# Kernel optimization log

Hardware: AMD Instinct MI355X
Metric: run time of the kernel (lower is better)

## Reference

```python
import jax, jax.numpy as jnp
import numpy as np

N = 100000   # nodes
E = 600000   # edges
G = 512      # graphs in batch
EPS = 1e-5   # LayerNorm eps
IN_DIM = 60 + 2 + 12  # dyn feats*frames + dims + st embedding
H = 128


def setup_inputs() -> dict:
    key = jax.random.key(0)
    ks = jax.random.split(key, 32)
    inp = {
        "x": jax.random.normal(ks[0], (N, 60), jnp.float32),
        "xdims": jax.random.uniform(ks[1], (N, 2), jnp.float32),
        "xsttype": jax.random.randint(ks[2], (N,), 0, 256, jnp.int32),
        "edge_index": jax.random.randint(ks[3], (2, E), 0, N, jnp.int32),
        "batch": jnp.sort(jax.random.randint(ks[4], (N,), 0, G, jnp.int32)),
        "emb": jax.random.normal(ks[5], (256, 12), jnp.float32),
    }
    def lin(k, i, o):
        s = 1.0 / np.sqrt(i)
        return jax.random.uniform(k, (i, o), jnp.float32, -s, s)
    dims = [IN_DIM, H, H]
    for l in range(2):
        i, o = dims[l], dims[l + 1]
        inp[f"Wl{l}"] = lin(ks[6 + 4 * l], i, o)   # lin_l: applied to aggregated neighbors
        inp[f"bl{l}"] = jnp.zeros((o,), jnp.float32)
        inp[f"Wr{l}"] = lin(ks[7 + 4 * l], i, o)   # lin_r: applied to root (no bias, PyG SAGEConv)
        inp[f"g{l}"] = jnp.ones((o,), jnp.float32)   # LayerNorm gamma
        inp[f"bn{l}"] = jnp.zeros((o,), jnp.float32)  # LayerNorm beta
    ld = [2 * H, 50, 50, 10]
    for l in range(3):
        inp[f"Wf{l}"] = lin(ks[20 + l], ld[l], ld[l + 1])
        inp[f"bf{l}"] = jnp.zeros((ld[l + 1],), jnp.float32)
    return inp


def _layer_norm(h, g, b):
    mu = jnp.mean(h, axis=-1, keepdims=True)
    var = jnp.mean(jnp.square(h - mu), axis=-1, keepdims=True)
    return (h - mu) * jax.lax.rsqrt(var + EPS) * g + b


def reference(x, xdims, xsttype, edge_index, batch, emb,
              Wl0, bl0, Wr0, g0, bn0,
              Wl1, bl1, Wr1, g1, bn1,
              Wf0, bf0, Wf1, bf1, Wf2, bf2):
    # node feature assembly: [N, 60+2+12]
    h = jnp.concatenate([x, xdims, emb[xsttype]], axis=1)

    src, dst = edge_index[0], edge_index[1]
    deg = jax.ops.segment_sum(jnp.ones((E,), h.dtype), dst, num_segments=N)
    inv_deg = (1.0 / jnp.maximum(deg, 1.0))[:, None]

    for Wl, bl, Wr, g, bn in ((Wl0, bl0, Wr0, g0, bn0), (Wl1, bl1, Wr1, g1, bn1)):
        # SAGEConv (mean aggr): out = lin_l(mean_j x_j) + lin_r(x_i)
        agg = jax.ops.segment_sum(h[src], dst, num_segments=N) * inv_deg
        h = agg @ Wl + bl + h @ Wr
        h = jax.nn.relu(_layer_norm(h, g, bn))  # dropout inactive (eval)

    # global mean / max pooling over graphs
    cnt = jax.ops.segment_sum(jnp.ones((N,), h.dtype), batch, num_segments=G)
    xmean = jax.ops.segment_sum(h, batch, num_segments=G) / jnp.maximum(cnt, 1.0)[:, None]
    xmax = jax.ops.segment_max(h, batch, num_segments=G)
    z = jnp.concatenate([xmean, xmax], axis=1)  # [G, 2H]

    for Wf, bf in ((Wf0, bf0), (Wf1, bf1), (Wf2, bf2)):
        z = jax.nn.relu(z @ Wf + bf)  # Linear + ReLU + Dropout(eval)
    return z
```

## Files before the change

kernel.cpp:

```cpp
#include <hip/hip_runtime.h>

#define NN 100000
#define NP 100096
#define NT (NP / 32)
#define EE 600000
#define GG 512
#define LN_EPS 1e-5f

typedef __attribute__((ext_vector_type(8))) __bf16 bf16x8;
typedef __attribute__((ext_vector_type(4))) float f32x4;

__device__ __forceinline__ unsigned short f2bf(float f) {
    unsigned int u = __float_as_uint(f);
    u = (u + 0x7fffu + ((u >> 16) & 1u)) >> 16;
    return (unsigned short)u;
}
__device__ __forceinline__ unsigned int pack2(float a, float b) {
    return (unsigned int)f2bf(a) | ((unsigned int)f2bf(b) << 16);
}
__device__ __forceinline__ void acc8(float* s, uint4 v) {
    s[0] += __uint_as_float(v.x << 16);
    s[1] += __uint_as_float(v.x & 0xffff0000u);
    s[2] += __uint_as_float(v.y << 16);
    s[3] += __uint_as_float(v.y & 0xffff0000u);
    s[4] += __uint_as_float(v.z << 16);
    s[5] += __uint_as_float(v.z & 0xffff0000u);
    s[6] += __uint_as_float(v.w << 16);
    s[7] += __uint_as_float(v.w & 0xffff0000u);
}

#define PREP_A (NP * 10)
#define PREP_W0 (128 * 160)
#define PREP_W1 (128 * 256)
#define PREP_WF (50 * 256 + 50 * 50 + 50 * 10)
#define PREP_TOT (PREP_A + PREP_W0 + PREP_W1 + PREP_WF + EE)

__global__ __launch_bounds__(256) void prep_kernel(
    const float* __restrict__ x, const float* __restrict__ xdims,
    const int* __restrict__ stt, const float* __restrict__ emb,
    const int* __restrict__ ei,
    const float* __restrict__ Wl0, const float* __restrict__ Wr0,
    const float* __restrict__ Wl1, const float* __restrict__ Wr1,
    const float* __restrict__ Wf0, const float* __restrict__ Wf1,
    const float* __restrict__ Wf2,
    unsigned short* __restrict__ H0r,
    unsigned short* __restrict__ Wt0, unsigned short* __restrict__ Wt1,
    float* __restrict__ W0T, float* __restrict__ W1T, float* __restrict__ W2T,
    int* __restrict__ deg)
{
    int idx = blockIdx.x * 256 + threadIdx.x;
    if (idx < PREP_A) {
        int node = idx / 10;
        int c8 = (idx - node * 10) * 8;
        unsigned short vals[8];
        if (node < NN) {
            int st = stt[node];
            #pragma unroll
            for (int i = 0; i < 8; ++i) {
                int f = c8 + i;
                float v = 0.f;
                if (f < 60)      v = x[node * 60 + f];
                else if (f < 62) v = xdims[node * 2 + (f - 60)];
                else if (f < 74) v = emb[st * 12 + (f - 62)];
                vals[i] = f2bf(v);
            }
        } else {
            #pragma unroll
            for (int i = 0; i < 8; ++i) vals[i] = 0;
        }
        uint4 o;
        o.x = (unsigned)vals[0] | ((unsigned)vals[1] << 16);
        o.y = (unsigned)vals[2] | ((unsigned)vals[3] << 16);
        o.z = (unsigned)vals[4] | ((unsigned)vals[5] << 16);
        o.w = (unsigned)vals[6] | ((unsigned)vals[7] << 16);
        *(uint4*)(H0r + (size_t)node * 80 + c8) = o;
    } else if (idx < PREP_A + PREP_W0) {
        int j = idx - PREP_A;
        int n = j / 160, k = j - n * 160;
        float v = 0.f;
        if (k < 74)                  v = Wl0[k * 128 + n];
        else if (k >= 80 && k < 154) v = Wr0[(k - 80) * 128 + n];
        Wt0[(size_t)n * 160 + k] = f2bf(v);
    } else if (idx < PREP_A + PREP_W0 + PREP_W1) {
        int j = idx - PREP_A - PREP_W0;
        int n = j >> 8, k = j & 255;
        float v = (k < 128) ? Wl1[k * 128 + n] : Wr1[(k - 128) * 128 + n];
        Wt1[(size_t)n * 256 + k] = f2bf(v);
    } else if (idx < PREP_A + PREP_W0 + PREP_W1 + PREP_WF) {
        int j = idx - PREP_A - PREP_W0 - PREP_W1;
        if (j < 50 * 256) {
            int t = j >> 8, k = j & 255;
            W0T[t * 256 + k] = Wf0[k * 50 + t];
        } else if (j < 50 * 256 + 50 * 50) {
            int q = j - 50 * 256; int t = q / 50, k = q - t * 50;
            W1T[t * 50 + k] = Wf1[k * 50 + t];
        } else {
            int q = j - 50 * 256 - 50 * 50; int t = q / 50, k = q - t * 50;
            W2T[t * 50 + k] = Wf2[k * 10 + t];
        }
    } else if (idx < PREP_TOT) {
        int e = idx - PREP_A - PREP_W0 - PREP_W1 - PREP_WF;
        atomicAdd(&deg[ei[EE + e]], 1);
    }
}

__global__ __launch_bounds__(256) void scan1_kernel(
    const int* __restrict__ deg, int* __restrict__ offs, int* __restrict__ bsum)
{
    __shared__ int ts[256];
    int t = threadIdx.x;
    int base = blockIdx.x * 2048 + t * 8;
    int d[8];
    if (base + 8 <= NN) {
        int4 a = *(const int4*)&deg[base];
        int4 b = *(const int4*)&deg[base + 4];
        d[0]=a.x; d[1]=a.y; d[2]=a.z; d[3]=a.w;
        d[4]=b.x; d[5]=b.y; d[6]=b.z; d[7]=b.w;
    } else {
        #pragma unroll
        for (int i = 0; i < 8; ++i) d[i] = (base + i < NN) ? deg[base + i] : 0;
    }
    int e[8]; int run = 0;
    #pragma unroll
    for (int i = 0; i < 8; ++i) { e[i] = run; run += d[i]; }
    ts[t] = run;
    int tot = run;
    __syncthreads();
    for (int off = 1; off < 256; off <<= 1) {
        int u = (t >= off) ? ts[t - off] : 0;
        __syncthreads();
        ts[t] += u;
        __syncthreads();
    }
    int pre = ts[t] - tot;
    #pragma unroll
    for (int i = 0; i < 8; ++i) if (base + i < NN) offs[base + i] = e[i] + pre;
    if (t == 255) bsum[blockIdx.x] = ts[255];
}

__global__ void scan2_kernel(int* __restrict__ bsum, int nb)
{
    int t = threadIdx.x;
    int v = (t < nb) ? bsum[t] : 0;
    int inc = v;
    for (int off = 1; off < 64; off <<= 1) {
        int u = __shfl_up(inc, off, 64);
        if (t >= off) inc += u;
    }
    if (t < nb) bsum[t] = inc - v;
}

__global__ __launch_bounds__(256) void fill_csr_kernel(
    const int* __restrict__ ei, int* __restrict__ cur,
    const int* __restrict__ offs, const int* __restrict__ bsum,
    int* __restrict__ csr)
{
    int e = blockIdx.x * 256 + threadIdx.x;
    if (e >= EE) return;
    int d = ei[EE + e];
    int p = offs[d] + bsum[d >> 11] + atomicAdd(&cur[d], 1);
    csr[p] = ei[e];
}

template<int K, bool POOL>
__global__ __launch_bounds__(256, 4) void gemm_kernel(
    const unsigned short* __restrict__ Hr,
    const unsigned short* __restrict__ Wt,
    const float* __restrict__ bias, const float* __restrict__ gamma,
    const float* __restrict__ beta,
    unsigned short* __restrict__ outH,
    const int* __restrict__ batch,
    float* __restrict__ psum, int* __restrict__ pmax, int* __restrict__ gcnt,
    const int* __restrict__ csr, const int* __restrict__ offs,
    const int* __restrict__ bsum, const int* __restrict__ deg)
{
    constexpr int KT = K / 32, AS = K + 8, KH = K / 2, CH = KH / 8;
    constexpr int SMEM = (32 * AS * 2 > 32 * 128 * 4) ? 32 * AS * 2 : 32 * 128 * 4;
    __shared__ __align__(16) char smem[SMEM];
    unsigned short* Asm = (unsigned short*)smem;
    float* Hs = (float*)smem;
    __shared__ __align__(16) float sP[32 * 4];
    __shared__ __align__(16) float qP[32 * 4];
    __shared__ int bS[POOL ? 32 : 1];

    const int tid = threadIdx.x;
    const int n0 = blockIdx.x * 32;
    const int l = tid & 63, w = tid >> 6;
    const int fg = l >> 4, c0 = l & 15;

    if (POOL && tid < 32) {
        int gn = n0 + tid;
        bS[tid] = (gn < NN) ? batch[gn] : -1;
    }
    float bia[2], gam[2], bet[2];
    #pragma unroll
    for (int j = 0; j < 2; ++j) {
        int col = (2 * w + j) * 16 + c0;
        bia[j] = bias[col]; gam[j] = gamma[col]; bet[j] = beta[col];
    }
    const unsigned short* bp0 = Wt + (size_t)((2 * w + 0) * 16 + c0) * K + fg * 8;
    const unsigned short* bp1 = Wt + (size_t)((2 * w + 1) * 16 + c0) * K + fg * 8;

    {
        const int ln = tid & 15, nl = tid >> 4;
        #pragma unroll
        for (int half = 0; half < 2; ++half) {
            int node = half * 16 + nl;
            int gn = n0 + node;
            if (ln < CH) {
                uint4 rv = *(const uint4*)(Hr + (size_t)gn * KH + ln * 8);
                int d = 0, st = 0;
                if (gn < NN) { d = deg[gn]; st = offs[gn] + bsum[gn >> 11]; }
                float iv = 1.0f / (float)(d > 1 ? d : 1);
                float s[8];
                #pragma unroll
                for (int i = 0; i < 8; ++i) s[i] = 0.f;
                int e = 0;
                for (; e + 4 <= d; e += 4) {
                    int i0 = csr[st + e],     i1 = csr[st + e + 1];
                    int i2 = csr[st + e + 2], i3 = csr[st + e + 3];
                    uint4 v0 = *(const uint4*)(Hr + (size_t)i0 * KH + ln * 8);
                    uint4 v1 = *(const uint4*)(Hr + (size_t)i1 * KH + ln * 8);
                    uint4 v2 = *(const uint4*)(Hr + (size_t)i2 * KH + ln * 8);
                    uint4 v3 = *(const uint4*)(Hr + (size_t)i3 * KH + ln * 8);
                    acc8(s, v0); acc8(s, v1); acc8(s, v2); acc8(s, v3);
                }
                for (; e < d; ++e) {
                    int i0 = csr[st + e];
                    uint4 v0 = *(const uint4*)(Hr + (size_t)i0 * KH + ln * 8);
                    acc8(s, v0);
                }
                uint4 o;
                o.x = pack2(s[0] * iv, s[1] * iv);
                o.y = pack2(s[2] * iv, s[3] * iv);
                o.z = pack2(s[4] * iv, s[5] * iv);
                o.w = pack2(s[6] * iv, s[7] * iv);
                *(uint4*)(Asm + node * AS + ln * 8) = o;
                *(uint4*)(Asm + node * AS + KH + ln * 8) = rv;
            }
        }
    }

    const unsigned short* ar0 = Asm + (0 * 16 + c0) * AS + fg * 8;
    const unsigned short* ar1 = Asm + (1 * 16 + c0) * AS + fg * 8;
    __syncthreads();

    f32x4 acc[2][2];
    acc[0][0] = (f32x4){0.f,0.f,0.f,0.f}; acc[0][1] = (f32x4){0.f,0.f,0.f,0.f};
    acc[1][0] = (f32x4){0.f,0.f,0.f,0.f}; acc[1][1] = (f32x4){0.f,0.f,0.f,0.f};

    #pragma unroll
    for (int kt = 0; kt < KT; ++kt) {
        bf16x8 b0 = *(const bf16x8*)(bp0 + kt * 32);
        bf16x8 b1 = *(const bf16x8*)(bp1 + kt * 32);
        bf16x8 a0 = *(const bf16x8*)(ar0 + kt * 32);
        bf16x8 a1 = *(const bf16x8*)(ar1 + kt * 32);
        acc[0][0] = __builtin_amdgcn_mfma_f32_16x16x32_bf16(a0, b0, acc[0][0], 0, 0, 0);
        acc[0][1] = __builtin_amdgcn_mfma_f32_16x16x32_bf16(a0, b1, acc[0][1], 0, 0, 0);
        acc[1][0] = __builtin_amdgcn_mfma_f32_16x16x32_bf16(a1, b0, acc[1][0], 0, 0, 0);
        acc[1][1] = __builtin_amdgcn_mfma_f32_16x16x32_bf16(a1, b1, acc[1][1], 0, 0, 0);
    }

    #pragma unroll
    for (int m = 0; m < 2; ++m) {
        #pragma unroll
        for (int r = 0; r < 4; ++r) {
            float h0v = acc[m][0][r] + bia[0];
            float h1v = acc[m][1][r] + bia[1];
            float s = h0v + h1v, q = h0v * h0v + h1v * h1v;
            #pragma unroll
            for (int mm = 1; mm < 16; mm <<= 1) {
                s += __shfl_xor(s, mm, 64);
                q += __shfl_xor(q, mm, 64);
            }
            if (c0 == 0) {
                int node = m * 16 + fg * 4 + r;
                sP[node * 4 + w] = s;
                qP[node * 4 + w] = q;
            }
        }
    }
    __syncthreads();

    #pragma unroll
    for (int m = 0; m < 2; ++m) {
        #pragma unroll
        for (int r = 0; r < 4; ++r) {
            int node = m * 16 + fg * 4 + r;
            float4 sv = *(const float4*)&sP[node * 4];
            float4 qv = *(const float4*)&qP[node * 4];
            float s = (sv.x + sv.y) + (sv.z + sv.w);
            float q = (qv.x + qv.y) + (qv.z + qv.w);
            float mu   = s * (1.f / 128.f);
            float var  = q * (1.f / 128.f) - mu * mu;
            float rinv = rsqrtf(var + LN_EPS);
            float h0v = acc[m][0][r] + bia[0];
            float h1v = acc[m][1][r] + bia[1];
            float v0 = fmaxf(0.f, (h0v - mu) * rinv * gam[0] + bet[0]);
            float v1 = fmaxf(0.f, (h1v - mu) * rinv * gam[1] + bet[1]);
            if (POOL) {
                Hs[node * 128 + (2 * w) * 16 + c0]     = v0;
                Hs[node * 128 + (2 * w + 1) * 16 + c0] = v1;
            } else {
                size_t gn = (size_t)(n0 + node);
                float keep = (gn < (size_t)NN) ? 1.f : 0.f;
                outH[gn * 128 + (2 * w) * 16 + c0]     = f2bf(v0 * keep);
                outH[gn * 128 + (2 * w + 1) * 16 + c0] = f2bf(v1 * keep);
            }
        }
    }
    if (!POOL) return;
    __syncthreads();

    if (tid < 128) {
        int j = tid;
        int curg = -1; float s = 0.f, m = 0.f; int rl = 0;
        #pragma unroll 4
        for (int n = 0; n < 32; ++n) {
            int gb = bS[n];
            if (gb < 0) break;
            if (gb != curg) {
                if (curg >= 0) {
                    atomicAdd(&psum[curg * 128 + j], s);
                    atomicMax(&pmax[curg * 128 + j], __float_as_int(m));
                    if (j == 0) atomicAdd(&gcnt[curg], rl);
                }
                curg = gb; s = 0.f; m = 0.f; rl = 0;
            }
            float v = Hs[n * 128 + j];
            s += v; m = fmaxf(m, v);
            rl += 1;
        }
        if (curg >= 0) {
            atomicAdd(&psum[curg * 128 + j], s);
            atomicMax(&pmax[curg * 128 + j], __float_as_int(m));
            if (j == 0) atomicAdd(&gcnt[curg], rl);
        }
    }
}

__global__ __launch_bounds__(64) void mlp_kernel(
    const float* __restrict__ psum, const int* __restrict__ pmax,
    const int* __restrict__ gcnt,
    const float* __restrict__ W0T, const float* __restrict__ bf0,
    const float* __restrict__ W1T, const float* __restrict__ bf1,
    const float* __restrict__ W2T, const float* __restrict__ bf2,
    float* __restrict__ out)
{
    __shared__ float z[256];
    __shared__ float t1[50];
    __shared__ float t2[50];
    int g = blockIdx.x, t = threadIdx.x;
    int c = gcnt[g];
    float ic = 1.0f / (float)(c > 1 ? c : 1);
    for (int j = t; j < 128; j += 64) {
        z[j]       = psum[g * 128 + j] * ic;
        z[128 + j] = __int_as_float(pmax[g * 128 + j]);
    }
    __syncthreads();
    if (t < 50) {
        const float* wr = W0T + t * 256;
        float a0 = bf0[t], a1 = 0.f, a2 = 0.f, a3 = 0.f;
        for (int k = 0; k < 256; k += 4) {
            float4 wv = *(const float4*)(wr + k);
            a0 = fmaf(z[k],     wv.x, a0);
            a1 = fmaf(z[k + 1], wv.y, a1);
            a2 = fmaf(z[k + 2], wv.z, a2);
            a3 = fmaf(z[k + 3], wv.w, a3);
        }
        t1[t] = fmaxf((a0 + a1) + (a2 + a3), 0.0f);
    }
    __syncthreads();
    if (t < 50) {
        const float* wr = W1T + t * 50;
        float a0 = bf1[t], a1 = 0.f;
        for (int k = 0; k < 50; k += 2) {
            a0 = fmaf(t1[k],     wr[k],     a0);
            a1 = fmaf(t1[k + 1], wr[k + 1], a1);
        }
        t2[t] = fmaxf(a0 + a1, 0.0f);
    }
    __syncthreads();
    if (t < 10) {
        const float* wr = W2T + t * 50;
        float a0 = bf2[t], a1 = 0.f;
        for (int k = 0; k < 50; k += 2) {
            a0 = fmaf(t2[k],     wr[k],     a0);
            a1 = fmaf(t2[k + 1], wr[k + 1], a1);
        }
        out[g * 10 + t] = fmaxf(a0 + a1, 0.0f);
    }
}

extern "C" void kernel_launch(void* const* d_in, const int* in_sizes, int n_in,
                              void* d_out, int out_size, void* d_ws, size_t ws_size,
                              hipStream_t stream)
{
    const float* x     = (const float*)d_in[0];
    const float* xdims = (const float*)d_in[1];
    const int*   stt   = (const int*)d_in[2];
    const int*   ei    = (const int*)d_in[3];
    const int*   batch = (const int*)d_in[4];
    const float* emb   = (const float*)d_in[5];
    const float* Wl0   = (const float*)d_in[6];
    const float* bl0   = (const float*)d_in[7];
    const float* Wr0   = (const float*)d_in[8];
    const float* g0    = (const float*)d_in[9];
    const float* bn0   = (const float*)d_in[10];
    const float* Wl1   = (const float*)d_in[11];
    const float* bl1   = (const float*)d_in[12];
    const float* Wr1   = (const float*)d_in[13];
    const float* g1    = (const float*)d_in[14];
    const float* bn1   = (const float*)d_in[15];
    const float* Wf0   = (const float*)d_in[16];
    const float* bf0   = (const float*)d_in[17];
    const float* Wf1   = (const float*)d_in[18];
    const float* bf1   = (const float*)d_in[19];
    const float* Wf2   = (const float*)d_in[20];
    const float* bf2   = (const float*)d_in[21];

    char* w = (char*)d_ws;
    unsigned short* H0r = (unsigned short*)w; w += (size_t)NP * 80 * 2;
    unsigned short* H1  = (unsigned short*)w; w += (size_t)NP * 128 * 2;
    unsigned short* Wt0 = (unsigned short*)w; w += (size_t)128 * 160 * 2;
    unsigned short* Wt1 = (unsigned short*)w; w += (size_t)128 * 256 * 2;
    float* W0T = (float*)w; w += (size_t)50 * 256 * 4;
    float* W1T = (float*)w; w += (size_t)50 * 50 * 4;
    float* W2T = (float*)w; w += (size_t)10 * 50 * 4;
    int*   csr    = (int*)w;   w += (size_t)EE * 4;
    int*   offs   = (int*)w;   w += (size_t)NN * 4;
    int*   bsum   = (int*)w;   w += 1024;
    char* zbeg = w;
    int*   deg  = (int*)w;   w += (size_t)NP * 4;
    int*   cur  = (int*)w;   w += (size_t)NN * 4;
    float* psum = (float*)w; w += (size_t)GG * 128 * 4;
    int*   pmax = (int*)w;   w += (size_t)GG * 128 * 4;
    int*   gcnt = (int*)w;   w += (size_t)GG * 4;
    size_t zsz = (size_t)(w - zbeg);

    hipMemsetAsync(zbeg, 0, zsz, stream);

    prep_kernel<<<(PREP_TOT + 255) / 256, 256, 0, stream>>>(
        x, xdims, stt, emb, ei, Wl0, Wr0, Wl1, Wr1, Wf0, Wf1, Wf2,
        H0r, Wt0, Wt1, W0T, W1T, W2T, deg);

    int nb = (NN + 2047) / 2048;
    scan1_kernel<<<nb, 256, 0, stream>>>(deg, offs, bsum);
    scan2_kernel<<<1, 64, 0, stream>>>(bsum, nb);
    fill_csr_kernel<<<(EE + 255) / 256, 256, 0, stream>>>(ei, cur, offs, bsum, csr);

    gemm_kernel<160, false><<<NT, 256, 0, stream>>>(
        H0r, Wt0, bl0, g0, bn0, H1, nullptr, nullptr, nullptr, nullptr,
        csr, offs, bsum, deg);
    gemm_kernel<256, true><<<NT, 256, 0, stream>>>(
        H1, Wt1, bl1, g1, bn1, nullptr, batch, psum, pmax, gcnt,
        csr, offs, bsum, deg);

    mlp_kernel<<<GG, 64, 0, stream>>>(psum, pmax, gcnt, W0T, bf0, W1T, bf1, W2T, bf2,
                                      (float*)d_out);
}
```

Before: 277.8 us.

## Partition degree count and CSR fill by destination range to localize atomics

The degree-count atomics in prep and the CSR fill kernel now have each edge chunk read by 8 blocks. Each block only handles destinations inside its own 12500-node partition. The aim is to keep the atomic targets and scattered writes of concurrently running blocks within a narrower address range, for better cache and L2 locality, and to vectorize the edge-index loads. The cost is that every edge-index chunk is read 8 times and most lanes idle through the branch checks.

```diff
diff --git a/kernel.cpp b/kernel.cpp
--- a/kernel.cpp
+++ b/kernel.cpp
@@ -33,7 +33,15 @@
 #define PREP_W0 (128 * 160)
 #define PREP_W1 (128 * 256)
 #define PREP_WF (50 * 256 + 50 * 50 + 50 * 10)
-#define PREP_TOT (PREP_A + PREP_W0 + PREP_W1 + PREP_WF + EE)
+#define PREP_AB   (PREP_A / 256)
+#define PREP_W0B  (PREP_W0 / 256)
+#define PREP_W1B  (PREP_W1 / 256)
+#define PREP_WFB  ((PREP_WF + 255) / 256)
+#define PREP_FIXED_B (PREP_AB + PREP_W0B + PREP_W1B + PREP_WFB)
+#define ECHUNK 2048
+#define NCHUNK ((EE + ECHUNK - 1) / ECHUNK)
+#define PREP_GRID (PREP_FIXED_B + NCHUNK * 8)
+#define PART 12500
 
 __global__ __launch_bounds__(256) void prep_kernel(
     const float* __restrict__ x, const float* __restrict__ xdims,
@@ -48,7 +56,28 @@
     float* __restrict__ W0T, float* __restrict__ W1T, float* __restrict__ W2T,
     int* __restrict__ deg)
 {
-    int idx = blockIdx.x * 256 + threadIdx.x;
+    int blk = blockIdx.x;
+    if (blk >= PREP_FIXED_B) {
+        int eb = blk - PREP_FIXED_B;
+        int px = eb & 7, c = eb >> 3;
+        int lo = px * PART, hi = lo + PART;
+        int base = c * ECHUNK + threadIdx.x * 8;
+        int d[8]; int n = 0;
+        if (base + 8 <= EE) {
+            int4 a = *(const int4*)&ei[EE + base];
+            int4 b = *(const int4*)&ei[EE + base + 4];
+            d[0]=a.x; d[1]=a.y; d[2]=a.z; d[3]=a.w;
+            d[4]=b.x; d[5]=b.y; d[6]=b.z; d[7]=b.w;
+            n = 8;
+        } else {
+            for (int u = 0; u < 8 && base + u < EE; ++u) d[u] = ei[EE + base + u];
+            n = (base < EE) ? (EE - base < 8 ? EE - base : 8) : 0;
+        }
+        for (int u = 0; u < n; ++u)
+            if (d[u] >= lo && d[u] < hi) atomicAdd(&deg[d[u]], 1);
+        return;
+    }
+    int idx = blk * 256 + threadIdx.x;
     if (idx < PREP_A) {
         int node = idx / 10;
         int c8 = (idx - node * 10) * 8;
@@ -86,7 +115,7 @@
         int n = j >> 8, k = j & 255;
         float v = (k < 128) ? Wl1[k * 128 + n] : Wr1[(k - 128) * 128 + n];
         Wt1[(size_t)n * 256 + k] = f2bf(v);
-    } else if (idx < PREP_A + PREP_W0 + PREP_W1 + PREP_WF) {
+    } else {
         int j = idx - PREP_A - PREP_W0 - PREP_W1;
         if (j < 50 * 256) {
             int t = j >> 8, k = j & 255;
@@ -94,13 +123,10 @@
         } else if (j < 50 * 256 + 50 * 50) {
             int q = j - 50 * 256; int t = q / 50, k = q - t * 50;
             W1T[t * 50 + k] = Wf1[k * 50 + t];
-        } else {
+        } else if (j < PREP_WF) {
             int q = j - 50 * 256 - 50 * 50; int t = q / 50, k = q - t * 50;
             W2T[t * 50 + k] = Wf2[k * 10 + t];
         }
-    } else if (idx < PREP_TOT) {
-        int e = idx - PREP_A - PREP_W0 - PREP_W1 - PREP_WF;
-        atomicAdd(&deg[ei[EE + e]], 1);
     }
 }
 
@@ -155,11 +181,27 @@
     const int* __restrict__ offs, const int* __restrict__ bsum,
     int* __restrict__ csr)
 {
-    int e = blockIdx.x * 256 + threadIdx.x;
-    if (e >= EE) return;
-    int d = ei[EE + e];
-    int p = offs[d] + bsum[d >> 11] + atomicAdd(&cur[d], 1);
-    csr[p] = ei[e];
+    int px = blockIdx.x & 7, c = blockIdx.x >> 3;
+    int lo = px * PART, hi = lo + PART;
+    int base = c * ECHUNK + threadIdx.x * 8;
+    int d[8]; int n = 0;
+    if (base + 8 <= EE) {
+        int4 a = *(const int4*)&ei[EE + base];
+        int4 b = *(const int4*)&ei[EE + base + 4];
+        d[0]=a.x; d[1]=a.y; d[2]=a.z; d[3]=a.w;
+        d[4]=b.x; d[5]=b.y; d[6]=b.z; d[7]=b.w;
+        n = 8;
+    } else {
+        for (int u = 0; u < 8 && base + u < EE; ++u) d[u] = ei[EE + base + u];
+        n = (base < EE) ? (EE - base < 8 ? EE - base : 8) : 0;
+    }
+    for (int u = 0; u < n; ++u) {
+        int dd = d[u];
+        if (dd >= lo && dd < hi) {
+            int p = offs[dd] + bsum[dd >> 11] + atomicAdd(&cur[dd], 1);
+            csr[p] = ei[base + u];
+        }
+    }
 }
 
 template<int K, bool POOL>
@@ -440,14 +482,14 @@
 
     hipMemsetAsync(zbeg, 0, zsz, stream);
 
-    prep_kernel<<<(PREP_TOT + 255) / 256, 256, 0, stream>>>(
+    prep_kernel<<<PREP_GRID, 256, 0, stream>>>(
         x, xdims, stt, emb, ei, Wl0, Wr0, Wl1, Wr1, Wf0, Wf1, Wf2,
         H0r, Wt0, Wt1, W0T, W1T, W2T, deg);
 
     int nb = (NN + 2047) / 2048;
     scan1_kernel<<<nb, 256, 0, stream>>>(deg, offs, bsum);
     scan2_kernel<<<1, 64, 0, stream>>>(bsum, nb);
-    fill_csr_kernel<<<(EE + 255) / 256, 256, 0, stream>>>(ei, cur, offs, bsum, csr);
+    fill_csr_kernel<<<NCHUNK * 8, 256, 0, stream>>>(ei, cur, offs, bsum, csr);
 
     gemm_kernel<160, false><<<NT, 256, 0, stream>>>(
         H0r, Wt0, bl0, g0, bn0, H1, nullptr, nullptr, nullptr, nullptr,
```

After: 279.0 us. About the same (+0.4%).
